# Kernel tuning notes

Measured on AMD Instinct MI355X. Metric: run time of the kernel, lower is better.

The kernel has to match this reference:

```python
import jax, jax.numpy as jnp
import numpy as np
import math

B, H, S, D = 4, 16, 2048, 64

def setup_inputs() -> dict:
    key = jax.random.key(0)
    kq, kk, kv = jax.random.split(key, 3)
    Q = jax.random.normal(kq, (B, H, S, D), dtype=jnp.float32)
    K = jax.random.normal(kk, (B, H, S, D), dtype=jnp.float32)
    V = jax.random.normal(kv, (B, H, S, D), dtype=jnp.float32)
    # causal mask, broadcast to [B, H, S, S] as the module expects '... queries keys'
    causal = jnp.tril(jnp.ones((S, S), dtype=bool))
    mask = jnp.broadcast_to(causal, (B, H, S, S))
    return {"Q": Q, "K": K, "V": V, "mask": mask}

def reference(Q, K, V, mask):
    d_k = Q.shape[-1]
    # [B,H,S_q,S_k] scores
    qk = jnp.einsum('bhqd,bhkd->bhqk', Q, K) / math.sqrt(d_k)
    qk = jnp.where(mask, qk, -jnp.inf)
    sm = jax.nn.softmax(qk, axis=-1)
    return jnp.einsum('bhqk,bhkd->bhqd', sm, V)
```

## Files before the change

kernel.cpp:

```cpp
#include <hip/hip_runtime.h>

#define SEQ  2048
#define DH   64
#define QBLK 128
#define KBLK 64
#define NQB  (SEQ/QBLK)
#define NTIL (SEQ/KBLK)
#define THR  11.5f
#define KPAT(r) ((((r)&3)) + 8*((r)>>2))
#define WS_NEEDED ((size_t)2 * 64 * SEQ * DH * 2)

typedef short bf16x8 __attribute__((ext_vector_type(8)));
typedef float f32x16 __attribute__((ext_vector_type(16)));

union V4U { unsigned int w[4]; bf16x8 v; };

__device__ __forceinline__ short bfbits(float f) {
    unsigned int u = __float_as_uint(f);
    u += 0x7fff + ((u >> 16) & 1);
    return (short)(u >> 16);
}
__device__ __forceinline__ unsigned int cvtpk(float lo, float hi) {
    unsigned int r;
    asm("v_cvt_pk_bf16_f32 %0, %1, %2" : "=v"(r) : "v"(lo), "v"(hi));
    return r;
}
__device__ __forceinline__ int swz(int row, int col) {
    return row * 64 + (col ^ ((row & 7) << 3));
}
__device__ __forceinline__ void gload16(const void* g, void* l) {
    __builtin_amdgcn_global_load_lds(
        (const __attribute__((address_space(1))) unsigned int*)g,
        (__attribute__((address_space(3))) unsigned int*)l,
        16, 0, 0);
}

__global__ __launch_bounds__(256) void prep_kv(const float* __restrict__ Kg,
                                               const float* __restrict__ Vg,
                                               short* __restrict__ Kimg,
                                               short* __restrict__ Vimg) {
    __shared__ __align__(16) short Vt[64 * 64];
    const int tid = threadIdx.x;
    const int t   = blockIdx.x & (NTIL - 1);
    const int bh  = blockIdx.x / NTIL;
    const int kb  = t * KBLK;

    const float* Kb = Kg + (size_t)bh * SEQ * DH;
    const float* Vb = Vg + (size_t)bh * SEQ * DH;
    short* kim = Kimg + ((size_t)bh * NTIL + t) * 4096;
    short* vim = Vimg + ((size_t)bh * NTIL + t) * 4096;

    {
        const int kr = tid >> 2, sd0 = (tid & 3) * 16;
        const float* src = Kb + (size_t)(kb + kr) * DH + sd0;
        const float4 a0 = *reinterpret_cast<const float4*>(src);
        const float4 a1 = *reinterpret_cast<const float4*>(src + 4);
        const float4 a2 = *reinterpret_cast<const float4*>(src + 8);
        const float4 a3 = *reinterpret_cast<const float4*>(src + 12);
        V4U u0, u1;
        u0.w[0] = cvtpk(a0.x, a0.y); u0.w[1] = cvtpk(a0.z, a0.w);
        u0.w[2] = cvtpk(a1.x, a1.y); u0.w[3] = cvtpk(a1.z, a1.w);
        u1.w[0] = cvtpk(a2.x, a2.y); u1.w[1] = cvtpk(a2.z, a2.w);
        u1.w[2] = cvtpk(a3.x, a3.y); u1.w[3] = cvtpk(a3.z, a3.w);
        *reinterpret_cast<bf16x8*>(&kim[swz(kr, sd0)])     = u0.v;
        *reinterpret_cast<bf16x8*>(&kim[swz(kr, sd0 + 8)]) = u1.v;
    }
    {
        const int vk = tid & 63, vd0 = (tid >> 6) * 16;
        const float* src = Vb + (size_t)(kb + vk) * DH + vd0;
        const float4 b0 = *reinterpret_cast<const float4*>(src);
        const float4 b1 = *reinterpret_cast<const float4*>(src + 4);
        const float4 b2 = *reinterpret_cast<const float4*>(src + 8);
        const float4 b3 = *reinterpret_cast<const float4*>(src + 12);
        const float vv[16] = {b0.x,b0.y,b0.z,b0.w, b1.x,b1.y,b1.z,b1.w,
                              b2.x,b2.y,b2.z,b2.w, b3.x,b3.y,b3.z,b3.w};
        #pragma unroll
        for (int i = 0; i < 16; ++i)
            Vt[swz(vd0 + i, vk)] = bfbits(vv[i]);
    }
    __syncthreads();
    *reinterpret_cast<bf16x8*>(&vim[tid * 16])     = *reinterpret_cast<const bf16x8*>(&Vt[tid * 16]);
    *reinterpret_cast<bf16x8*>(&vim[tid * 16 + 8]) = *reinterpret_cast<const bf16x8*>(&Vt[tid * 16 + 8]);
}

#define STAGE(b_, t_) do {                                                   \
    const short* kim_ = kimg + (size_t)(t_) * 4096 + w * 1024 + lane * 8;    \
    const short* vim_ = vimg + (size_t)(t_) * 4096 + w * 1024 + lane * 8;    \
    gload16(kim_,       &Ks[b_][w * 1024]);                                  \
    gload16(kim_ + 512, &Ks[b_][w * 1024 + 512]);                            \
    gload16(vim_,       &Vt[b_][w * 1024]);                                  \
    gload16(vim_ + 512, &Vt[b_][w * 1024 + 512]);                            \
} while (0)

__device__ __forceinline__ void tile_compute(
    const short* __restrict__ Ksb, const short* __restrict__ Vtb,
    int kb, int kend, int qw, int q, int h, int ql,
    const bf16x8 (&qb)[4], f32x16& o0, f32x16& o1, float& m, float& lsum)
{
    if (kb >= kend) return;
    const bool v2 = (kb + 32 < kend);

    f32x16 sT0, sT1;
    #pragma unroll
    for (int i = 0; i < 16; ++i) sT0[i] = 0.f;
    __builtin_amdgcn_s_setprio(1);
    #pragma unroll
    for (int dc = 0; dc < 4; ++dc) {
        const bf16x8 ka = *reinterpret_cast<const bf16x8*>(&Ksb[swz(ql, dc * 16 + h * 8)]);
        sT0 = __builtin_amdgcn_mfma_f32_32x32x16_bf16(ka, qb[dc], sT0, 0, 0, 0);
    }
    __builtin_amdgcn_s_setprio(0);
    if (v2) {
        #pragma unroll
        for (int i = 0; i < 16; ++i) sT1[i] = 0.f;
        __builtin_amdgcn_s_setprio(1);
        #pragma unroll
        for (int dc = 0; dc < 4; ++dc) {
            const bf16x8 ka = *reinterpret_cast<const bf16x8*>(&Ksb[swz(32 + ql, dc * 16 + h * 8)]);
            sT1 = __builtin_amdgcn_mfma_f32_32x32x16_bf16(ka, qb[dc], sT1, 0, 0, 0);
        }
        __builtin_amdgcn_s_setprio(0);
    }

    if (kb + 31 > qw) {
        #pragma unroll
        for (int r = 0; r < 16; ++r)
            if (kb + KPAT(r) + 4 * h > q) sT0[r] = -1e30f;
    }
    if (v2 && (kb + 63 > qw)) {
        #pragma unroll
        for (int r = 0; r < 16; ++r)
            if (kb + 32 + KPAT(r) + 4 * h > q) sT1[r] = -1e30f;
    }

    float mx = sT0[0];
    #pragma unroll
    for (int r = 1; r < 16; ++r) mx = fmaxf(mx, sT0[r]);
    if (v2) {
        #pragma unroll
        for (int r = 0; r < 16; ++r) mx = fmaxf(mx, sT1[r]);
    }
    if (!__all(mx <= m + THR)) {
        mx = fmaxf(mx, __shfl_xor(mx, 32));
        const float mn  = fmaxf(m, mx);
        const float scl = __builtin_amdgcn_exp2f(m - mn);
        m = mn;
        lsum *= scl;
        #pragma unroll
        for (int r = 0; r < 16; ++r) {
            const float sr = __shfl(scl, KPAT(r) + 4 * h);
            o0[r] *= sr; o1[r] *= sr;
        }
    }

    bf16x8 pa[4];
    {
        float p0[16];
        #pragma unroll
        for (int r = 0; r < 16; ++r) p0[r] = __builtin_amdgcn_exp2f(sT0[r] - m);
        #pragma unroll
        for (int r = 0; r < 16; ++r) lsum += p0[r];
        #pragma unroll
        for (int oct = 0; oct < 2; ++oct) {
            const unsigned int A0 = cvtpk(p0[oct*8+0], p0[oct*8+1]);
            const unsigned int A1 = cvtpk(p0[oct*8+2], p0[oct*8+3]);
            const unsigned int B0 = cvtpk(p0[oct*8+4], p0[oct*8+5]);
            const unsigned int B1 = cvtpk(p0[oct*8+6], p0[oct*8+7]);
            const unsigned int s0 = h ? A0 : B0, s1 = h ? A1 : B1;
            const unsigned int r0 = (unsigned int)__shfl_xor((int)s0, 32);
            const unsigned int r1 = (unsigned int)__shfl_xor((int)s1, 32);
            V4U u;
            u.w[0] = h ? r0 : A0; u.w[1] = h ? r1 : A1;
            u.w[2] = h ? B0 : r0; u.w[3] = h ? B1 : r1;
            pa[oct] = u.v;
        }
    }
    if (v2) {
        float p1[16];
        #pragma unroll
        for (int r = 0; r < 16; ++r) p1[r] = __builtin_amdgcn_exp2f(sT1[r] - m);
        #pragma unroll
        for (int r = 0; r < 16; ++r) lsum += p1[r];
        #pragma unroll
        for (int oct = 0; oct < 2; ++oct) {
            const unsigned int A0 = cvtpk(p1[oct*8+0], p1[oct*8+1]);
            const unsigned int A1 = cvtpk(p1[oct*8+2], p1[oct*8+3]);
            const unsigned int B0 = cvtpk(p1[oct*8+4], p1[oct*8+5]);
            const unsigned int B1 = cvtpk(p1[oct*8+6], p1[oct*8+7]);
            const unsigned int s0 = h ? A0 : B0, s1 = h ? A1 : B1;
            const unsigned int r0 = (unsigned int)__shfl_xor((int)s0, 32);
            const unsigned int r1 = (unsigned int)__shfl_xor((int)s1, 32);
            V4U u;
            u.w[0] = h ? r0 : A0; u.w[1] = h ? r1 : A1;
            u.w[2] = h ? B0 : r0; u.w[3] = h ? B1 : r1;
            pa[2 + oct] = u.v;
        }
    }

    __builtin_amdgcn_s_setprio(1);
    #pragma unroll
    for (int kt = 0; kt < 2; ++kt) {
        const bf16x8 vb0 = *reinterpret_cast<const bf16x8*>(&Vtb[swz(ql,      kt * 16 + h * 8)]);
        const bf16x8 vb1 = *reinterpret_cast<const bf16x8*>(&Vtb[swz(32 + ql, kt * 16 + h * 8)]);
        o0 = __builtin_amdgcn_mfma_f32_32x32x16_bf16(pa[kt], vb0, o0, 0, 0, 0);
        o1 = __builtin_amdgcn_mfma_f32_32x32x16_bf16(pa[kt], vb1, o1, 0, 0, 0);
    }
    __builtin_amdgcn_s_setprio(0);
    if (v2) {
        __builtin_amdgcn_s_setprio(1);
        #pragma unroll
        for (int kt = 2; kt < 4; ++kt) {
            const bf16x8 vb0 = *reinterpret_cast<const bf16x8*>(&Vtb[swz(ql,      kt * 16 + h * 8)]);
            const bf16x8 vb1 = *reinterpret_cast<const bf16x8*>(&Vtb[swz(32 + ql, kt * 16 + h * 8)]);
            o0 = __builtin_amdgcn_mfma_f32_32x32x16_bf16(pa[kt], vb0, o0, 0, 0, 0);
            o1 = __builtin_amdgcn_mfma_f32_32x32x16_bf16(pa[kt], vb1, o1, 0, 0, 0);
        }
        __builtin_amdgcn_s_setprio(0);
    }
}

__device__ __forceinline__ void load_qfrags(const float* Qb, int q, int h, float SC,
                                            bf16x8 (&qb)[4]) {
    const float* qp = Qb + (size_t)q * DH + h * 8;
    #pragma unroll
    for (int dc = 0; dc < 4; ++dc) {
        const float4 a = *reinterpret_cast<const float4*>(qp + dc * 16);
        const float4 b = *reinterpret_cast<const float4*>(qp + dc * 16 + 4);
        V4U u;
        u.w[0] = cvtpk(a.x * SC, a.y * SC);
        u.w[1] = cvtpk(a.z * SC, a.w * SC);
        u.w[2] = cvtpk(b.x * SC, b.y * SC);
        u.w[3] = cvtpk(b.z * SC, b.w * SC);
        qb[dc] = u.v;
    }
}

__device__ __forceinline__ void epilogue_store(float* Ob, int qw, int h, int ql,
                                               const f32x16& o0, const f32x16& o1,
                                               float lsum) {
    lsum += __shfl_xor(lsum, 32);
    const float inv = 1.0f / lsum;
    #pragma unroll
    for (int r = 0; r < 16; ++r) {
        const float ir  = __shfl(inv, KPAT(r) + 4 * h);
        const size_t row = (size_t)(qw + KPAT(r) + 4 * h);
        Ob[row * DH + ql]      = o0[r] * ir;
        Ob[row * DH + 32 + ql] = o1[r] * ir;
    }
}

__global__ __launch_bounds__(256, 2) void attn_fwd(const float* __restrict__ Qg,
                                                   const short* __restrict__ Kimg,
                                                   const short* __restrict__ Vimg,
                                                   float* __restrict__ Og) {
    __shared__ __align__(16) short Ks[3][64 * 64];
    __shared__ __align__(16) short Vt[3][64 * 64];

    const int tid  = threadIdx.x;
    const int w    = tid >> 6;
    const int lane = tid & 63;
    const int h    = lane >> 5;
    const int ql   = lane & 31;

    const int p   = blockIdx.x & 7;
    const int bh  = blockIdx.x >> 3;
    const int qblkA = p, qblkB = NQB - 1 - p;

    const float* Qb   = Qg + (size_t)bh * SEQ * DH;
    const short* kimg = Kimg + (size_t)bh * NTIL * 4096;
    const short* vimg = Vimg + (size_t)bh * NTIL * 4096;
    float*       Ob   = Og + (size_t)bh * SEQ * DH;

    const float SC = 0.125f * 1.44269504f;

    const int qwA = qblkA * QBLK + w * 32, qA = qwA + ql, kendA = qwA + 32;
    const int qwB = qblkB * QBLK + w * 32, qB = qwB + ql, kendB = qwB + 32;
    const int nt  = qblkB * 2 + 2;

    STAGE(0, 0);
    STAGE(1, 1);

    bf16x8 qbA[4], qbB[4];
    load_qfrags(Qb, qA, h, SC, qbA);
    load_qfrags(Qb, qB, h, SC, qbB);

    f32x16 oA0, oA1, oB0, oB1;
    #pragma unroll
    for (int i = 0; i < 16; ++i) { oA0[i]=0.f; oA1[i]=0.f; oB0[i]=0.f; oB1[i]=0.f; }
    float mA = -1e30f, lA = 0.f, mB = -1e30f, lB = 0.f;

    __syncthreads();

    for (int t = 0; t < nt; ++t) {
        const int kb  = t * KBLK;
        const int cur = t % 3;

        if (t + 1 < nt) asm volatile("s_waitcnt vmcnt(4)" ::: "memory");
        else            asm volatile("s_waitcnt vmcnt(0)" ::: "memory");
        __builtin_amdgcn_s_barrier();
        __builtin_amdgcn_sched_barrier(0);

        if (t + 2 < nt) STAGE((t + 2) % 3, t + 2);

        tile_compute(&Ks[cur][0], &Vt[cur][0], kb, kendA, qwA, qA, h, ql,
                     qbA, oA0, oA1, mA, lA);
        tile_compute(&Ks[cur][0], &Vt[cur][0], kb, kendB, qwB, qB, h, ql,
                     qbB, oB0, oB1, mB, lB);
    }

    epilogue_store(Ob, qwA, h, ql, oA0, oA1, lA);
    epilogue_store(Ob, qwB, h, ql, oB0, oB1, lB);
}

#define LOAD_STAGE(kb_) do {                                               \
    const float* ksrc = Kb + (size_t)((kb_) + skr) * DH + sd0;             \
    kr0 = *reinterpret_cast<const float4*>(ksrc);                          \
    kr1 = *reinterpret_cast<const float4*>(ksrc + 4);                      \
    kr2 = *reinterpret_cast<const float4*>(ksrc + 8);                      \
    kr3 = *reinterpret_cast<const float4*>(ksrc + 12);                     \
    const float* vsrc = Vb + (size_t)((kb_) + svk) * DH + svd0;            \
    vr0 = *reinterpret_cast<const float4*>(vsrc);                          \
    vr1 = *reinterpret_cast<const float4*>(vsrc + 4);                      \
    vr2 = *reinterpret_cast<const float4*>(vsrc + 8);                      \
    vr3 = *reinterpret_cast<const float4*>(vsrc + 12);                     \
} while (0)

#define CVT_WRITE(b_) do {                                                 \
    V4U u0, u1;                                                            \
    u0.w[0] = cvtpk(kr0.x, kr0.y); u0.w[1] = cvtpk(kr0.z, kr0.w);          \
    u0.w[2] = cvtpk(kr1.x, kr1.y); u0.w[3] = cvtpk(kr1.z, kr1.w);          \
    u1.w[0] = cvtpk(kr2.x, kr2.y); u1.w[1] = cvtpk(kr2.z, kr2.w);          \
    u1.w[2] = cvtpk(kr3.x, kr3.y); u1.w[3] = cvtpk(kr3.z, kr3.w);          \
    *reinterpret_cast<bf16x8*>(&Ks[b_][swz(skr, sd0)])     = u0.v;         \
    *reinterpret_cast<bf16x8*>(&Ks[b_][swz(skr, sd0 + 8)]) = u1.v;         \
    const float vv[16] = {vr0.x,vr0.y,vr0.z,vr0.w, vr1.x,vr1.y,vr1.z,vr1.w,\
                          vr2.x,vr2.y,vr2.z,vr2.w, vr3.x,vr3.y,vr3.z,vr3.w};\
    _Pragma("unroll")                                                      \
    for (int i_ = 0; i_ < 16; ++i_)                                        \
        Vt[b_][swz(svd0 + i_, svk)] = bfbits(vv[i_]);                      \
} while (0)

__global__ __launch_bounds__(256) void attn_fwd_fb(const float* __restrict__ Qg,
                                                   const float* __restrict__ Kg,
                                                   const float* __restrict__ Vg,
                                                   float* __restrict__ Og) {
    __shared__ __align__(16) short Ks[2][64 * 64];
    __shared__ __align__(16) short Vt[2][64 * 64];

    const int tid  = threadIdx.x;
    const int w    = tid >> 6;
    const int lane = tid & 63;
    const int h    = lane >> 5;
    const int ql   = lane & 31;

    const int j    = blockIdx.x & (NQB - 1);
    const int bh   = blockIdx.x / NQB;
    const int qblk = ((bh >> 4) & 1) ? (NQB - 1 - j) : j;
    const int q0   = qblk * QBLK;
    const int qw   = q0 + w * 32;
    const int q    = qw + ql;

    const float* Qb = Qg + (size_t)bh * SEQ * DH;
    const float* Kb = Kg + (size_t)bh * SEQ * DH;
    const float* Vb = Vg + (size_t)bh * SEQ * DH;
    float*       Ob = Og + (size_t)bh * SEQ * DH;

    const float SC = 0.125f * 1.44269504f;

    const int skr  = tid >> 2;
    const int sd0  = (tid & 3) * 16;
    const int svk  = tid & 63;
    const int svd0 = (tid >> 6) * 16;

    float4 kr0, kr1, kr2, kr3, vr0, vr1, vr2, vr3;
    LOAD_STAGE(0);

    bf16x8 qb[4];
    load_qfrags(Qb, q, h, SC, qb);

    f32x16 o0, o1;
    #pragma unroll
    for (int i = 0; i < 16; ++i) { o0[i] = 0.f; o1[i] = 0.f; }
    float m = -1e30f, lsum = 0.f;

    CVT_WRITE(0);
    __syncthreads();

    const int kend = qw + 32;
    const int nt   = (q0 + QBLK) / KBLK;

    for (int t = 0; t < nt; ++t) {
        const int kb  = t * KBLK;
        const int cur = t & 1;
        if (t + 1 < nt) LOAD_STAGE(kb + KBLK);

        tile_compute(&Ks[cur][0], &Vt[cur][0], kb, kend, qw, q, h, ql,
                     qb, o0, o1, m, lsum);

        if (t + 1 < nt) CVT_WRITE(cur ^ 1);
        __syncthreads();
    }

    epilogue_store(Ob, qw, h, ql, o0, o1, lsum);
}

extern "C" void kernel_launch(void* const* d_in, const int* in_sizes, int n_in,
                              void* d_out, int out_size, void* d_ws, size_t ws_size,
                              hipStream_t stream) {
    const float* Q = (const float*)d_in[0];
    const float* K = (const float*)d_in[1];
    const float* V = (const float*)d_in[2];
    float* O = (float*)d_out;

    if (ws_size >= WS_NEEDED) {
        short* Kimg = (short*)d_ws;
        short* Vimg = Kimg + (size_t)64 * NTIL * 4096;
        prep_kv<<<dim3(64 * NTIL), 256, 0, stream>>>(K, V, Kimg, Vimg);
        attn_fwd<<<dim3(64 * (NQB / 2)), 256, 0, stream>>>(Q, Kimg, Vimg, O);
    } else {
        attn_fwd_fb<<<dim3(64 * NQB), 256, 0, stream>>>(Q, K, V, O);
    }
}
```

Baseline: 85.80 us.

## Share K/V LDS fragments across both query blocks and interleave QK phases

```diff
diff --git a/kernel.cpp b/kernel.cpp
--- a/kernel.cpp
+++ b/kernel.cpp
@@ -83,62 +83,61 @@
     *reinterpret_cast<bf16x8*>(&vim[tid * 16 + 8]) = *reinterpret_cast<const bf16x8*>(&Vt[tid * 16 + 8]);
 }
 
-#define STAGE(b_, t_) do {                                                   \
-    const short* kim_ = kimg + (size_t)(t_) * 4096 + w * 1024 + lane * 8;    \
-    const short* vim_ = vimg + (size_t)(t_) * 4096 + w * 1024 + lane * 8;    \
-    gload16(kim_,       &Ks[b_][w * 1024]);                                  \
-    gload16(kim_ + 512, &Ks[b_][w * 1024 + 512]);                            \
-    gload16(vim_,       &Vt[b_][w * 1024]);                                  \
-    gload16(vim_ + 512, &Vt[b_][w * 1024 + 512]);                            \
-} while (0)
-
-__device__ __forceinline__ void tile_compute(
-    const short* __restrict__ Ksb, const short* __restrict__ Vtb,
-    int kb, int kend, int qw, int q, int h, int ql,
-    const bf16x8 (&qb)[4], f32x16& o0, f32x16& o1, float& m, float& lsum)
-{
-    if (kb >= kend) return;
-    const bool v2 = (kb + 32 < kend);
-
-    f32x16 sT0, sT1;
-    #pragma unroll
-    for (int i = 0; i < 16; ++i) sT0[i] = 0.f;
+__device__ __forceinline__ void load_kf8(const short* __restrict__ Ksb, int ql, int h,
+                                         bf16x8 (&kf)[8]) {
+    #pragma unroll
+    for (int dc = 0; dc < 4; ++dc) {
+        kf[dc]     = *reinterpret_cast<const bf16x8*>(&Ksb[swz(ql,      dc * 16 + h * 8)]);
+        kf[4 + dc] = *reinterpret_cast<const bf16x8*>(&Ksb[swz(32 + ql, dc * 16 + h * 8)]);
+    }
+}
+__device__ __forceinline__ void load_vf8(const short* __restrict__ Vtb, int ql, int h,
+                                         bf16x8 (&vf)[8]) {
+    #pragma unroll
+    for (int kt = 0; kt < 4; ++kt) {
+        vf[kt]     = *reinterpret_cast<const bf16x8*>(&Vtb[swz(ql,      kt * 16 + h * 8)]);
+        vf[4 + kt] = *reinterpret_cast<const bf16x8*>(&Vtb[swz(32 + ql, kt * 16 + h * 8)]);
+    }
+}
+__device__ __forceinline__ void qk_phase(const bf16x8 (&kf)[8], const bf16x8 (&qb)[4],
+                                         f32x16& s0, f32x16& s1, bool v2) {
+    #pragma unroll
+    for (int i = 0; i < 16; ++i) s0[i] = 0.f;
     __builtin_amdgcn_s_setprio(1);
     #pragma unroll
-    for (int dc = 0; dc < 4; ++dc) {
-        const bf16x8 ka = *reinterpret_cast<const bf16x8*>(&Ksb[swz(ql, dc * 16 + h * 8)]);
-        sT0 = __builtin_amdgcn_mfma_f32_32x32x16_bf16(ka, qb[dc], sT0, 0, 0, 0);
-    }
+    for (int dc = 0; dc < 4; ++dc)
+        s0 = __builtin_amdgcn_mfma_f32_32x32x16_bf16(kf[dc], qb[dc], s0, 0, 0, 0);
     __builtin_amdgcn_s_setprio(0);
     if (v2) {
         #pragma unroll
-        for (int i = 0; i < 16; ++i) sT1[i] = 0.f;
+        for (int i = 0; i < 16; ++i) s1[i] = 0.f;
         __builtin_amdgcn_s_setprio(1);
         #pragma unroll
-        for (int dc = 0; dc < 4; ++dc) {
-            const bf16x8 ka = *reinterpret_cast<const bf16x8*>(&Ksb[swz(32 + ql, dc * 16 + h * 8)]);
-            sT1 = __builtin_amdgcn_mfma_f32_32x32x16_bf16(ka, qb[dc], sT1, 0, 0, 0);
-        }
+        for (int dc = 0; dc < 4; ++dc)
+            s1 = __builtin_amdgcn_mfma_f32_32x32x16_bf16(kf[4 + dc], qb[dc], s1, 0, 0, 0);
         __builtin_amdgcn_s_setprio(0);
     }
-
+}
+__device__ __forceinline__ void sm_pack(f32x16& s0, f32x16& s1, bool v2,
+                                        int kb, int qw, int q, int h,
+                                        float& m, float& lsum,
+                                        f32x16& o0, f32x16& o1, bf16x8 (&pa)[4]) {
     if (kb + 31 > qw) {
         #pragma unroll
         for (int r = 0; r < 16; ++r)
-            if (kb + KPAT(r) + 4 * h > q) sT0[r] = -1e30f;
+            if (kb + KPAT(r) + 4 * h > q) s0[r] = -1e30f;
     }
     if (v2 && (kb + 63 > qw)) {
         #pragma unroll
         for (int r = 0; r < 16; ++r)
-            if (kb + 32 + KPAT(r) + 4 * h > q) sT1[r] = -1e30f;
-    }
-
-    float mx = sT0[0];
-    #pragma unroll
-    for (int r = 1; r < 16; ++r) mx = fmaxf(mx, sT0[r]);
+            if (kb + 32 + KPAT(r) + 4 * h > q) s1[r] = -1e30f;
+    }
+    float mx = s0[0];
+    #pragma unroll
+    for (int r = 1; r < 16; ++r) mx = fmaxf(mx, s0[r]);
     if (v2) {
         #pragma unroll
-        for (int r = 0; r < 16; ++r) mx = fmaxf(mx, sT1[r]);
+        for (int r = 0; r < 16; ++r) mx = fmaxf(mx, s1[r]);
     }
     if (!__all(mx <= m + THR)) {
         mx = fmaxf(mx, __shfl_xor(mx, 32));
@@ -152,71 +151,57 @@
             o0[r] *= sr; o1[r] *= sr;
         }
     }
-
-    bf16x8 pa[4];
-    {
-        float p0[16];
-        #pragma unroll
-        for (int r = 0; r < 16; ++r) p0[r] = __builtin_amdgcn_exp2f(sT0[r] - m);
-        #pragma unroll
-        for (int r = 0; r < 16; ++r) lsum += p0[r];
+    #pragma unroll
+    for (int r = 0; r < 16; ++r) { s0[r] = __builtin_amdgcn_exp2f(s0[r] - m); lsum += s0[r]; }
+    #pragma unroll
+    for (int oct = 0; oct < 2; ++oct) {
+        const unsigned int A0 = cvtpk(s0[oct*8+0], s0[oct*8+1]);
+        const unsigned int A1 = cvtpk(s0[oct*8+2], s0[oct*8+3]);
+        const unsigned int B0 = cvtpk(s0[oct*8+4], s0[oct*8+5]);
+        const unsigned int B1 = cvtpk(s0[oct*8+6], s0[oct*8+7]);
+        const unsigned int t0 = h ? A0 : B0, t1 = h ? A1 : B1;
+        const unsigned int r0 = (unsigned int)__shfl_xor((int)t0, 32);
+        const unsigned int r1 = (unsigned int)__shfl_xor((int)t1, 32);
+        V4U u;
+        u.w[0] = h ? r0 : A0; u.w[1] = h ? r1 : A1;
+        u.w[2] = h ? B0 : r0; u.w[3] = h ? B1 : r1;
+        pa[oct] = u.v;
+    }
+    if (v2) {
+        #pragma unroll
+        for (int r = 0; r < 16; ++r) { s1[r] = __builtin_amdgcn_exp2f(s1[r] - m); lsum += s1[r]; }
         #pragma unroll
         for (int oct = 0; oct < 2; ++oct) {
-            const unsigned int A0 = cvtpk(p0[oct*8+0], p0[oct*8+1]);
-            const unsigned int A1 = cvtpk(p0[oct*8+2], p0[oct*8+3]);
-            const unsigned int B0 = cvtpk(p0[oct*8+4], p0[oct*8+5]);
-            const unsigned int B1 = cvtpk(p0[oct*8+6], p0[oct*8+7]);
-            const unsigned int s0 = h ? A0 : B0, s1 = h ? A1 : B1;
-            const unsigned int r0 = (unsigned int)__shfl_xor((int)s0, 32);
-            const unsigned int r1 = (unsigned int)__shfl_xor((int)s1, 32);
-            V4U u;
-            u.w[0] = h ? r0 : A0; u.w[1] = h ? r1 : A1;
-            u.w[2] = h ? B0 : r0; u.w[3] = h ? B1 : r1;
-            pa[oct] = u.v;
-        }
-    }
-    if (v2) {
-        float p1[16];
-        #pragma unroll
-        for (int r = 0; r < 16; ++r) p1[r] = __builtin_amdgcn_exp2f(sT1[r] - m);
-        #pragma unroll
-        for (int r = 0; r < 16; ++r) lsum += p1[r];
-        #pragma unroll
-        for (int oct = 0; oct < 2; ++oct) {
-            const unsigned int A0 = cvtpk(p1[oct*8+0], p1[oct*8+1]);
-            const unsigned int A1 = cvtpk(p1[oct*8+2], p1[oct*8+3]);
-            const unsigned int B0 = cvtpk(p1[oct*8+4], p1[oct*8+5]);
-            const unsigned int B1 = cvtpk(p1[oct*8+6], p1[oct*8+7]);
-            const unsigned int s0 = h ? A0 : B0, s1 = h ? A1 : B1;
-            const unsigned int r0 = (unsigned int)__shfl_xor((int)s0, 32);
-            const unsigned int r1 = (unsigned int)__shfl_xor((int)s1, 32);
+            const unsigned int A0 = cvtpk(s1[oct*8+0], s1[oct*8+1]);
+            const unsigned int A1 = cvtpk(s1[oct*8+2], s1[oct*8+3]);
+            const unsigned int B0 = cvtpk(s1[oct*8+4], s1[oct*8+5]);
+            const unsigned int B1 = cvtpk(s1[oct*8+6], s1[oct*8+7]);
+            const unsigned int t0 = h ? A0 : B0, t1 = h ? A1 : B1;
+            const unsigned int r0 = (unsigned int)__shfl_xor((int)t0, 32);
+            const unsigned int r1 = (unsigned int)__shfl_xor((int)t1, 32);
             V4U u;
             u.w[0] = h ? r0 : A0; u.w[1] = h ? r1 : A1;
             u.w[2] = h ? B0 : r0; u.w[3] = h ? B1 : r1;
             pa[2 + oct] = u.v;
         }
     }
-
+}
+__device__ __forceinline__ void pv_phase(const bf16x8 (&pa)[4], const bf16x8 (&vf)[8],
+                                         f32x16& o0, f32x16& o1, bool v2) {
     __builtin_amdgcn_s_setprio(1);
     #pragma unroll
     for (int kt = 0; kt < 2; ++kt) {
-        const bf16x8 vb0 = *reinterpret_cast<const bf16x8*>(&Vtb[swz(ql,      kt * 16 + h * 8)]);
-        const bf16x8 vb1 = *reinterpret_cast<const bf16x8*>(&Vtb[swz(32 + ql, kt * 16 + h * 8)]);
-        o0 = __builtin_amdgcn_mfma_f32_32x32x16_bf16(pa[kt], vb0, o0, 0, 0, 0);
-        o1 = __builtin_amdgcn_mfma_f32_32x32x16_bf16(pa[kt], vb1, o1, 0, 0, 0);
+        o0 = __builtin_amdgcn_mfma_f32_32x32x16_bf16(pa[kt], vf[kt],     o0, 0, 0, 0);
+        o1 = __builtin_amdgcn_mfma_f32_32x32x16_bf16(pa[kt], vf[4 + kt], o1, 0, 0, 0);
+    }
+    if (v2) {
+        #pragma unroll
+        for (int kt = 2; kt < 4; ++kt) {
+            o0 = __builtin_amdgcn_mfma_f32_32x32x16_bf16(pa[kt], vf[kt],     o0, 0, 0, 0);
+            o1 = __builtin_amdgcn_mfma_f32_32x32x16_bf16(pa[kt], vf[4 + kt], o1, 0, 0, 0);
+        }
     }
     __builtin_amdgcn_s_setprio(0);
-    if (v2) {
-        __builtin_amdgcn_s_setprio(1);
-        #pragma unroll
-        for (int kt = 2; kt < 4; ++kt) {
-            const bf16x8 vb0 = *reinterpret_cast<const bf16x8*>(&Vtb[swz(ql,      kt * 16 + h * 8)]);
-            const bf16x8 vb1 = *reinterpret_cast<const bf16x8*>(&Vtb[swz(32 + ql, kt * 16 + h * 8)]);
-            o0 = __builtin_amdgcn_mfma_f32_32x32x16_bf16(pa[kt], vb0, o0, 0, 0, 0);
-            o1 = __builtin_amdgcn_mfma_f32_32x32x16_bf16(pa[kt], vb1, o1, 0, 0, 0);
-        }
-        __builtin_amdgcn_s_setprio(0);
-    }
 }
 
 __device__ __forceinline__ void load_qfrags(const float* Qb, int q, int h, float SC,
@@ -249,6 +234,15 @@
     }
 }
 
+#define STAGE(b_, t_) do {                                                   \
+    const short* kim_ = kimg + (size_t)(t_) * 4096 + w * 1024 + lane * 8;    \
+    const short* vim_ = vimg + (size_t)(t_) * 4096 + w * 1024 + lane * 8;    \
+    gload16(kim_,       &Ks[b_][w * 1024]);                                  \
+    gload16(kim_ + 512, &Ks[b_][w * 1024 + 512]);                            \
+    gload16(vim_,       &Vt[b_][w * 1024]);                                  \
+    gload16(vim_ + 512, &Vt[b_][w * 1024 + 512]);                            \
+} while (0)
+
 __global__ __launch_bounds__(256, 2) void attn_fwd(const float* __restrict__ Qg,
                                                    const short* __restrict__ Kimg,
                                                    const short* __restrict__ Vimg,
@@ -298,14 +292,36 @@
         if (t + 1 < nt) asm volatile("s_waitcnt vmcnt(4)" ::: "memory");
         else            asm volatile("s_waitcnt vmcnt(0)" ::: "memory");
         __builtin_amdgcn_s_barrier();
-        __builtin_amdgcn_sched_barrier(0);
 
         if (t + 2 < nt) STAGE((t + 2) % 3, t + 2);
 
-        tile_compute(&Ks[cur][0], &Vt[cur][0], kb, kendA, qwA, qA, h, ql,
-                     qbA, oA0, oA1, mA, lA);
-        tile_compute(&Ks[cur][0], &Vt[cur][0], kb, kendB, qwB, qB, h, ql,
-                     qbB, oB0, oB1, mB, lB);
+        const short* Ksb = &Ks[cur][0];
+        const short* Vtb = &Vt[cur][0];
+        const bool aAct = kb < kendA;
+        const bool bAct = kb < kendB;
+        const bool v2A  = kb + 32 < kendA;
+        const bool v2B  = kb + 32 < kendB;
+
+        bf16x8 kf[8];
+        load_kf8(Ksb, ql, h, kf);
+
+        f32x16 sA0, sA1, sB0, sB1;
+        if (aAct) qk_phase(kf, qbA, sA0, sA1, v2A);
+        if (bAct) qk_phase(kf, qbB, sB0, sB1, v2B);
+
+        bf16x8 vf[8];
+        load_vf8(Vtb, ql, h, vf);
+
+        if (aAct) {
+            bf16x8 paA[4];
+            sm_pack(sA0, sA1, v2A, kb, qwA, qA, h, mA, lA, oA0, oA1, paA);
+            pv_phase(paA, vf, oA0, oA1, v2A);
+        }
+        if (bAct) {
+            bf16x8 paB[4];
+            sm_pack(sB0, sB1, v2B, kb, qwB, qB, h, mB, lB, oB0, oB1, paB);
+            pv_phase(paB, vf, oB0, oB1, v2B);
+        }
     }
 
     epilogue_store(Ob, qwA, h, ql, oA0, oA1, lA);
@@ -394,9 +410,18 @@
         const int cur = t & 1;
         if (t + 1 < nt) LOAD_STAGE(kb + KBLK);
 
-        tile_compute(&Ks[cur][0], &Vt[cur][0], kb, kend, qw, q, h, ql,
-                     qb, o0, o1, m, lsum);
-
+        if (kb < kend) {
+            const bool v2 = (kb + 32 < kend);
+            bf16x8 kf[8];
+            load_kf8(&Ks[cur][0], ql, h, kf);
+            f32x16 s0, s1;
+            qk_phase(kf, qb, s0, s1, v2);
+            bf16x8 vf[8];
+            load_vf8(&Vt[cur][0], ql, h, vf);
+            bf16x8 pa[4];
+            sm_pack(s0, s1, v2, kb, qw, q, h, m, lsum, o0, o1, pa);
+            pv_phase(pa, vf, o0, o1, v2);
+        }
         if (t + 1 < nt) CVT_WRITE(cur ^ 1);
         __syncthreads();
     }
```

Result: no change. 86.09 us (+0.3%).
